# Kernel optimization log

Measured on AMD Instinct MI355X. Metric: run time of the kernel, lower is better.

Reference implementation:

```python
import jax, jax.numpy as jnp
import numpy as np

INPUT, HIDDEN, OUTPUT = 512, 512, 512


def setup_inputs() -> dict:
    key = jax.random.key(0)
    ks = jax.random.split(key, 8)
    B, T = 64, 1024
    s_x = 1.0 / np.sqrt(INPUT)
    s_h = 1.0 / np.sqrt(HIDDEN)
    return {
        "x": jax.random.normal(ks[0], (B, T, INPUT), jnp.float32),
        "h0": jnp.zeros((B, HIDDEN), jnp.float32),
        # nn.Linear params: weight (out, in), bias (out,), U(-1/sqrt(in), 1/sqrt(in))
        "W_xh": jax.random.uniform(ks[1], (HIDDEN, INPUT), jnp.float32, -s_x, s_x),
        "b_xh": jax.random.uniform(ks[2], (HIDDEN,), jnp.float32, -s_x, s_x),
        "W_hh": jax.random.uniform(ks[3], (HIDDEN, HIDDEN), jnp.float32, -s_h, s_h),
        "b_hh": jax.random.uniform(ks[4], (HIDDEN,), jnp.float32, -s_h, s_h),
        "W_hy": jax.random.uniform(ks[5], (OUTPUT, HIDDEN), jnp.float32, -s_h, s_h),
        "b_hy": jax.random.uniform(ks[6], (OUTPUT,), jnp.float32, -s_h, s_h),
    }


def reference(x, h0, W_xh, b_xh, W_hh, b_hh, W_hy, b_hy):
    # h_t = tanh(W_hh h_{t-1} + b_hh + W_xh x_t + b_xh); y_t = W_hy h_t + b_hy
    # Precompute the input projection for all timesteps (one big GEMM).
    xp = jnp.einsum("bti,hi->bth", x, W_xh) + b_xh + b_hh  # (B, T, H)

    def step(h, xp_t):
        h = jnp.tanh(h @ W_hh.T + xp_t)
        return h, h

    h_n, hs = jax.lax.scan(step, h0, jnp.swapaxes(xp, 0, 1))  # hs: (T, B, H)
    hs = jnp.swapaxes(hs, 0, 1)  # (B, T, H)
    output = jnp.einsum("bth,oh->bto", hs, W_hy) + b_hy
    return output, h_n
```

## Files before the change

kernel.cpp:

```cpp
#include <hip/hip_runtime.h>

typedef _Float16 f16;
typedef _Float16 f16x2 __attribute__((ext_vector_type(2)));
typedef _Float16 f16x4 __attribute__((ext_vector_type(4)));
typedef _Float16 f16x8 __attribute__((ext_vector_type(8)));
typedef float    f32x4 __attribute__((ext_vector_type(4)));

__device__ __forceinline__ int sdot4(int a, int b, int c) {
#if __has_builtin(__builtin_amdgcn_sdot4)
  return __builtin_amdgcn_sdot4(a, b, c, false);
#else
#pragma unroll
  for (int i = 0; i < 4; ++i)
    c += ((a << (24 - 8 * i)) >> 24) * ((b << (24 - 8 * i)) >> 24);
  return c;
#endif
}


__global__ void cvt_f32_to_f16(const float* __restrict__ in, f16* __restrict__ out, int n) {
  int i = (blockIdx.x * blockDim.x + threadIdx.x) * 4;
  if (i + 3 < n) {
    float4 v = *(const float4*)(in + i);
    f16x4 h; h[0] = (f16)v.x; h[1] = (f16)v.y; h[2] = (f16)v.z; h[3] = (f16)v.w;
    *(f16x4*)(out + i) = h;
  }
}

__global__ void bias_comb_kernel(const float* __restrict__ a, const float* __restrict__ b,
                                 float* __restrict__ o, int n) {
  int i = blockIdx.x * blockDim.x + threadIdx.x;
  if (i < n) o[i] = a[i] + b[i];
}

__global__ void zero_u32_kernel(unsigned* p) { *p = 0u; }

__global__ void wabsmax_kernel(const float* __restrict__ in, int n, unsigned* out) {
  float m = 0.f;
  for (int i = blockIdx.x * blockDim.x + threadIdx.x; i < n; i += gridDim.x * blockDim.x)
    m = fmaxf(m, fabsf(in[i]));
#pragma unroll
  for (int off = 32; off >= 1; off >>= 1)
    m = fmaxf(m, __shfl_xor(m, off));
  if ((threadIdx.x & 63) == 0) atomicMax(out, __float_as_uint(m));
}

__global__ void quant_w_kernel(const float* __restrict__ W, signed char* __restrict__ out,
                               const unsigned* __restrict__ wmax, int n) {
  float mx = __uint_as_float(*wmax);
  float inv = mx > 0.f ? 127.f / mx : 0.f;
  int i = (blockIdx.x * blockDim.x + threadIdx.x) * 4;
  if (i + 3 < n) {
    float4 v = *(const float4*)(W + i);
    int q0 = (int)__builtin_rintf(v.x * inv);
    int q1 = (int)__builtin_rintf(v.y * inv);
    int q2 = (int)__builtin_rintf(v.z * inv);
    int q3 = (int)__builtin_rintf(v.w * inv);
    unsigned p = (unsigned)(q0 & 255) | ((unsigned)(q1 & 255) << 8) |
                 ((unsigned)(q2 & 255) << 16) | ((unsigned)(q3 & 255) << 24);
    *(unsigned*)(out + i) = p;
  }
}


#define BM 128
#define BN 128
#define BKT 32
#define LDK 40

template <bool A_IS_F32>
__global__ __launch_bounds__(256, 2) void gemm_f16_kernel(
    const void* __restrict__ Aptr,
    const f16* __restrict__ B,
    const float* __restrict__ bias,
    float* __restrict__ C,
    int M, int N, int K) {
  __shared__ f16 As[BM][LDK];
  __shared__ f16 Bs[BN][LDK];

  const int tid = threadIdx.x;
  const int bm = blockIdx.y, bn = blockIdx.x;
  const int wave = tid >> 6, lane = tid & 63;
  const int wm = wave >> 1, wn = wave & 1;

  f32x4 acc[4][4] = {};

  for (int k0 = 0; k0 < K; k0 += BKT) {
#pragma unroll
    for (int it = 0; it < 2; ++it) {
      int idx = tid + it * 256;
      int row = idx >> 2;
      int kc  = (idx & 3) << 3;
      if (A_IS_F32) {
        const float* Af = (const float*)Aptr + (size_t)(bm * BM + row) * K + k0 + kc;
        float4 v0 = *(const float4*)Af;
        float4 v1 = *(const float4*)(Af + 4);
        f16x8 h;
        h[0] = (f16)v0.x; h[1] = (f16)v0.y; h[2] = (f16)v0.z; h[3] = (f16)v0.w;
        h[4] = (f16)v1.x; h[5] = (f16)v1.y; h[6] = (f16)v1.z; h[7] = (f16)v1.w;
        *(f16x8*)&As[row][kc] = h;
      } else {
        const f16* Ah = (const f16*)Aptr + (size_t)(bm * BM + row) * K + k0 + kc;
        *(f16x8*)&As[row][kc] = *(const f16x8*)Ah;
      }
      const f16* Bh = B + (size_t)(bn * BN + row) * K + k0 + kc;
      *(f16x8*)&Bs[row][kc] = *(const f16x8*)Bh;
    }
    __syncthreads();

    const int fr = lane & 15;
    const int fk = (lane >> 4) << 3;
    f16x8 af[4], bf[4];
#pragma unroll
    for (int i = 0; i < 4; ++i) af[i] = *(const f16x8*)&As[wm * 64 + i * 16 + fr][fk];
#pragma unroll
    for (int j = 0; j < 4; ++j) bf[j] = *(const f16x8*)&Bs[wn * 64 + j * 16 + fr][fk];
#pragma unroll
    for (int i = 0; i < 4; ++i)
#pragma unroll
      for (int j = 0; j < 4; ++j)
        acc[i][j] = __builtin_amdgcn_mfma_f32_16x16x32_f16(af[i], bf[j], acc[i][j], 0, 0, 0);
    __syncthreads();
  }

  const int fr = lane & 15;
  const int fq = lane >> 4;
#pragma unroll
  for (int i = 0; i < 4; ++i)
#pragma unroll
    for (int j = 0; j < 4; ++j)
#pragma unroll
      for (int r = 0; r < 4; ++r) {
        int row = bm * BM + wm * 64 + i * 16 + fq * 4 + r;
        int col = bn * BN + wn * 64 + j * 16 + fr;
        C[(size_t)row * N + col] = acc[i][j][r] + bias[col];
      }
}


#define RT 512

__global__ __launch_bounds__(RT, 1) void rnn_scan_kernel(
    const signed char* __restrict__ Whq,
    const unsigned* __restrict__ wmax,
    const float* __restrict__ h0,
    const float* __restrict__ xp,
    f16* __restrict__ hs,
    float* __restrict__ hn,
    int T) {
  __shared__ __align__(16) signed char hbuf[2][RT];
  const int tid = threadIdx.x;
  const int b   = blockIdx.x;

  const float qs = __uint_as_float(*wmax) * (1.0f / 16129.0f);

  const int* wrow = (const int*)(Whq + (size_t)tid * 512);
  int wq[128];
#pragma unroll
  for (int i = 0; i < 128; ++i) wq[i] = wrow[i];

  {
    float hv = h0[(size_t)b * 512 + tid];
    hv = fminf(1.f, fmaxf(-1.f, hv));
    hbuf[0][tid] = (signed char)(int)__builtin_rintf(127.f * hv);
  }
  __syncthreads();

  const float* xpb = xp + (size_t)b * T * 512 + tid;
  f16* hsb = hs + (size_t)b * T * 512 + tid;

  int cur = 0;
  float hlast = 0.f;
  float xv = xpb[0];
  for (int t = 0; t < T; ++t) {
    int tn = t + 1 < T ? t + 1 : t;
    float xn = xpb[(size_t)tn * 512];

    const int4* bcp = (const int4*)hbuf[cur];
    int a0 = 0, a1 = 0, a2 = 0, a3 = 0;
#pragma unroll
    for (int c = 0; c < 32; ++c) {
      int4 hv = bcp[c];
      a0 = sdot4(wq[4 * c + 0], hv.x, a0);
      a1 = sdot4(wq[4 * c + 1], hv.y, a1);
      a2 = sdot4(wq[4 * c + 2], hv.z, a2);
      a3 = sdot4(wq[4 * c + 3], hv.w, a3);
    }
    float acc = (float)((a0 + a1) + (a2 + a3)) * qs + xv;
    float e = __expf(2.0f * acc);
    float hnew = 1.0f - 2.0f * __builtin_amdgcn_rcpf(e + 1.0f);
    hlast = hnew;
    hsb[(size_t)t * 512] = (f16)hnew;
    hbuf[cur ^ 1][tid] = (signed char)(int)__builtin_rintf(127.f * hnew);
    __syncthreads();
    cur ^= 1;
    xv = xn;
  }
  hn[(size_t)b * 512 + tid] = hlast;
}


extern "C" void kernel_launch(void* const* d_in, const int* in_sizes, int n_in,
                              void* d_out, int out_size, void* d_ws, size_t ws_size,
                              hipStream_t stream) {
  const float* x    = (const float*)d_in[0];
  const float* h0   = (const float*)d_in[1];
  const float* W_xh = (const float*)d_in[2];
  const float* b_xh = (const float*)d_in[3];
  const float* W_hh = (const float*)d_in[4];
  const float* b_hh = (const float*)d_in[5];
  const float* W_hy = (const float*)d_in[6];
  const float* b_hy = (const float*)d_in[7];

  const int H = 512;
  const int B = in_sizes[1] / H;
  const int T = in_sizes[0] / (B * H);
  const int M = B * T;

  float* out = (float*)d_out;
  float* xpb = out;
  float* hn  = out + (size_t)M * H;

  char* w = (char*)d_ws;
  f16*         hsb    = (f16*)w;
  f16*         Wxh_h  = (f16*)(w + (size_t)M * H * 2);
  f16*         Why_h  = Wxh_h + H * H;
  signed char* Whq    = (signed char*)(Why_h + H * H);
  float*       biasc  = (float*)(Whq + H * H);
  unsigned*    wmax   = (unsigned*)(biasc + H);

  const int WN = H * H;
  cvt_f32_to_f16<<<WN / 1024, 256, 0, stream>>>(W_xh, Wxh_h, WN);
  cvt_f32_to_f16<<<WN / 1024, 256, 0, stream>>>(W_hy, Why_h, WN);
  bias_comb_kernel<<<2, 256, 0, stream>>>(b_xh, b_hh, biasc, H);

  zero_u32_kernel<<<1, 1, 0, stream>>>(wmax);
  wabsmax_kernel<<<64, 256, 0, stream>>>(W_hh, WN, wmax);
  quant_w_kernel<<<WN / 1024, 256, 0, stream>>>(W_hh, Whq, wmax, WN);

  gemm_f16_kernel<true><<<dim3(H / BN, M / BM), 256, 0, stream>>>(
      x, Wxh_h, biasc, xpb, M, H, H);

  rnn_scan_kernel<<<B, RT, 0, stream>>>(Whq, wmax, h0, xpb, hsb, hn, T);

  gemm_f16_kernel<false><<<dim3(H / BN, M / BM), 256, 0, stream>>>(
      hsb, Why_h, b_hy, out, M, H, H);
}
```

Measured before the change: 852.8 us.

## Split RNN scan K-dimension across two thread halves with LDS partial reduction

The recurrent scan block grows from 512 to 1024 threads, and each output neuron's 512-wide int8 dot product is split into two halves of 256. The upper half writes its partial sum to shared memory, and after a barrier the lower half adds it and computes the tanh update. This halves the serial sdot4 chain per step and the weight registers per thread (64 instead of 128), which allows more waves. The cost is an extra __syncthreads and an LDS round trip on every timestep of the latency-bound loop.

```diff
diff --git a/kernel.cpp b/kernel.cpp
--- a/kernel.cpp
+++ b/kernel.cpp
@@ -138,9 +138,18 @@
 }
 
 
-#define RT 512
-
-__global__ __launch_bounds__(RT, 1) void rnn_scan_kernel(
+#define ST 1024
+
+#define STEP_CHUNK(c, wa, wb, wcc, wd) \
+  { int4 hv = bcp[c];                  \
+    a0 = sdot4(wa, hv.x, a0);          \
+    a1 = sdot4(wb, hv.y, a1);          \
+    a2 = sdot4(wcc, hv.z, a2);         \
+    a3 = sdot4(wd, hv.w, a3); }
+
+__global__ __attribute__((amdgpu_flat_work_group_size(ST, ST),
+                          amdgpu_waves_per_eu(4, 4)))
+void rnn_scan_kernel(
     const signed char* __restrict__ Whq,
     const unsigned* __restrict__ wmax,
     const float* __restrict__ h0,
@@ -148,55 +157,98 @@
     f16* __restrict__ hs,
     float* __restrict__ hn,
     int T) {
-  __shared__ __align__(16) signed char hbuf[2][RT];
+  __shared__ __align__(16) signed char hbuf[2][512];
+  __shared__ int ipart[512];
+
   const int tid = threadIdx.x;
+  const int j   = tid & 511;
+  const int kh  = tid >> 9;
   const int b   = blockIdx.x;
 
   const float qs = __uint_as_float(*wmax) * (1.0f / 16129.0f);
 
-  const int* wrow = (const int*)(Whq + (size_t)tid * 512);
-  int wq[128];
-#pragma unroll
-  for (int i = 0; i < 128; ++i) wq[i] = wrow[i];
-
-  {
-    float hv = h0[(size_t)b * 512 + tid];
+  const int* wrow = (const int*)(Whq + (size_t)j * 512) + kh * 64;
+  int w0 =wrow[0],  w1 =wrow[1],  w2 =wrow[2],  w3 =wrow[3],
+      w4 =wrow[4],  w5 =wrow[5],  w6 =wrow[6],  w7 =wrow[7];
+  int w8 =wrow[8],  w9 =wrow[9],  w10=wrow[10], w11=wrow[11],
+      w12=wrow[12], w13=wrow[13], w14=wrow[14], w15=wrow[15];
+  int w16=wrow[16], w17=wrow[17], w18=wrow[18], w19=wrow[19],
+      w20=wrow[20], w21=wrow[21], w22=wrow[22], w23=wrow[23];
+  int w24=wrow[24], w25=wrow[25], w26=wrow[26], w27=wrow[27],
+      w28=wrow[28], w29=wrow[29], w30=wrow[30], w31=wrow[31];
+  int w32=wrow[32], w33=wrow[33], w34=wrow[34], w35=wrow[35],
+      w36=wrow[36], w37=wrow[37], w38=wrow[38], w39=wrow[39];
+  int w40=wrow[40], w41=wrow[41], w42=wrow[42], w43=wrow[43],
+      w44=wrow[44], w45=wrow[45], w46=wrow[46], w47=wrow[47];
+  int w48=wrow[48], w49=wrow[49], w50=wrow[50], w51=wrow[51],
+      w52=wrow[52], w53=wrow[53], w54=wrow[54], w55=wrow[55];
+  int w56=wrow[56], w57=wrow[57], w58=wrow[58], w59=wrow[59],
+      w60=wrow[60], w61=wrow[61], w62=wrow[62], w63=wrow[63];
+  asm volatile("" : "+v"(w0),"+v"(w1),"+v"(w2),"+v"(w3),"+v"(w4),"+v"(w5),"+v"(w6),"+v"(w7));
+  asm volatile("" : "+v"(w8),"+v"(w9),"+v"(w10),"+v"(w11),"+v"(w12),"+v"(w13),"+v"(w14),"+v"(w15));
+  asm volatile("" : "+v"(w16),"+v"(w17),"+v"(w18),"+v"(w19),"+v"(w20),"+v"(w21),"+v"(w22),"+v"(w23));
+  asm volatile("" : "+v"(w24),"+v"(w25),"+v"(w26),"+v"(w27),"+v"(w28),"+v"(w29),"+v"(w30),"+v"(w31));
+  asm volatile("" : "+v"(w32),"+v"(w33),"+v"(w34),"+v"(w35),"+v"(w36),"+v"(w37),"+v"(w38),"+v"(w39));
+  asm volatile("" : "+v"(w40),"+v"(w41),"+v"(w42),"+v"(w43),"+v"(w44),"+v"(w45),"+v"(w46),"+v"(w47));
+  asm volatile("" : "+v"(w48),"+v"(w49),"+v"(w50),"+v"(w51),"+v"(w52),"+v"(w53),"+v"(w54),"+v"(w55));
+  asm volatile("" : "+v"(w56),"+v"(w57),"+v"(w58),"+v"(w59),"+v"(w60),"+v"(w61),"+v"(w62),"+v"(w63));
+
+  if (kh == 0) {
+    float hv = h0[(size_t)b * 512 + j];
     hv = fminf(1.f, fmaxf(-1.f, hv));
-    hbuf[0][tid] = (signed char)(int)__builtin_rintf(127.f * hv);
+    hbuf[0][j] = (signed char)(int)__builtin_rintf(127.f * hv);
   }
   __syncthreads();
 
-  const float* xpb = xp + (size_t)b * T * 512 + tid;
-  f16* hsb = hs + (size_t)b * T * 512 + tid;
+  const float* xpb = xp + (size_t)b * T * 512 + j;
+  f16* hsb = hs + (size_t)b * T * 512 + j;
 
   int cur = 0;
   float hlast = 0.f;
-  float xv = xpb[0];
+  float xv = (kh == 0) ? xpb[0] : 0.f;
   for (int t = 0; t < T; ++t) {
-    int tn = t + 1 < T ? t + 1 : t;
-    float xn = xpb[(size_t)tn * 512];
-
-    const int4* bcp = (const int4*)hbuf[cur];
+    float xn = xv;
+    if (kh == 0) {
+      int tn = t + 1 < T ? t + 1 : t;
+      xn = xpb[(size_t)tn * 512];
+    }
+
+    const int4* bcp = (const int4*)hbuf[cur] + kh * 16;
     int a0 = 0, a1 = 0, a2 = 0, a3 = 0;
-#pragma unroll
-    for (int c = 0; c < 32; ++c) {
-      int4 hv = bcp[c];
-      a0 = sdot4(wq[4 * c + 0], hv.x, a0);
-      a1 = sdot4(wq[4 * c + 1], hv.y, a1);
-      a2 = sdot4(wq[4 * c + 2], hv.z, a2);
-      a3 = sdot4(wq[4 * c + 3], hv.w, a3);
+    STEP_CHUNK( 0, w0,  w1,  w2,  w3 )
+    STEP_CHUNK( 1, w4,  w5,  w6,  w7 )
+    STEP_CHUNK( 2, w8,  w9,  w10, w11)
+    STEP_CHUNK( 3, w12, w13, w14, w15)
+    STEP_CHUNK( 4, w16, w17, w18, w19)
+    STEP_CHUNK( 5, w20, w21, w22, w23)
+    STEP_CHUNK( 6, w24, w25, w26, w27)
+    STEP_CHUNK( 7, w28, w29, w30, w31)
+    STEP_CHUNK( 8, w32, w33, w34, w35)
+    STEP_CHUNK( 9, w36, w37, w38, w39)
+    STEP_CHUNK(10, w40, w41, w42, w43)
+    STEP_CHUNK(11, w44, w45, w46, w47)
+    STEP_CHUNK(12, w48, w49, w50, w51)
+    STEP_CHUNK(13, w52, w53, w54, w55)
+    STEP_CHUNK(14, w56, w57, w58, w59)
+    STEP_CHUNK(15, w60, w61, w62, w63)
+    int ai = (a0 + a1) + (a2 + a3);
+
+    if (kh == 1) ipart[j] = ai;
+    __syncthreads();
+
+    if (kh == 0) {
+      float acc = (float)(ai + ipart[j]) * qs + xv;
+      float e = __expf(2.0f * acc);
+      float hnew = 1.0f - 2.0f * __builtin_amdgcn_rcpf(e + 1.0f);
+      hlast = hnew;
+      hsb[(size_t)t * 512] = (f16)hnew;
+      hbuf[cur ^ 1][j] = (signed char)(int)__builtin_rintf(127.f * hnew);
     }
-    float acc = (float)((a0 + a1) + (a2 + a3)) * qs + xv;
-    float e = __expf(2.0f * acc);
-    float hnew = 1.0f - 2.0f * __builtin_amdgcn_rcpf(e + 1.0f);
-    hlast = hnew;
-    hsb[(size_t)t * 512] = (f16)hnew;
-    hbuf[cur ^ 1][tid] = (signed char)(int)__builtin_rintf(127.f * hnew);
     __syncthreads();
     cur ^= 1;
     xv = xn;
   }
-  hn[(size_t)b * 512 + tid] = hlast;
+  if (kh == 0) hn[(size_t)b * 512 + j] = hlast;
 }
 
 
@@ -241,7 +293,7 @@
   gemm_f16_kernel<true><<<dim3(H / BN, M / BM), 256, 0, stream>>>(
       x, Wxh_h, biasc, xpb, M, H, H);
 
-  rnn_scan_kernel<<<B, RT, 0, stream>>>(Whq, wmax, h0, xpb, hsb, hn, T);
+  rnn_scan_kernel<<<B, ST, 0, stream>>>(Whq, wmax, h0, xpb, hsb, hn, T);
 
   gemm_f16_kernel<false><<<dim3(H / BN, M / BM), 256, 0, stream>>>(
       hsb, Why_h, b_hy, out, M, H, H);
```

Measured after the change: 1.098 ms. +28.8%, slower.

## Use int8 MFMA for recurrent matvec in RNN scan kernel

Applied to the files above, without the earlier changes.

Replaces the per-thread sdot4 dot-product loop in the recurrent scan with v_mfma_i32_16x16x64_i8 instructions. Each wave keeps its slice of the quantized W_hh in AGPRs and reads the int8 hidden state from LDS as the A operand, broadcast across 16 rows. Only the first 16 lanes of each wave apply tanh and write outputs. Most of each MFMA tile is wasted because only one row is meaningful, and the hand-written s_nop hazard padding adds latency on every step.

```diff
diff --git a/kernel.cpp b/kernel.cpp
--- a/kernel.cpp
+++ b/kernel.cpp
@@ -5,17 +5,7 @@
 typedef _Float16 f16x4 __attribute__((ext_vector_type(4)));
 typedef _Float16 f16x8 __attribute__((ext_vector_type(8)));
 typedef float    f32x4 __attribute__((ext_vector_type(4)));
-
-__device__ __forceinline__ int sdot4(int a, int b, int c) {
-#if __has_builtin(__builtin_amdgcn_sdot4)
-  return __builtin_amdgcn_sdot4(a, b, c, false);
-#else
-#pragma unroll
-  for (int i = 0; i < 4; ++i)
-    c += ((a << (24 - 8 * i)) >> 24) * ((b << (24 - 8 * i)) >> 24);
-  return c;
-#endif
-}
+typedef int      intx4 __attribute__((ext_vector_type(4)));
 
 
 __global__ void cvt_f32_to_f16(const float* __restrict__ in, f16* __restrict__ out, int n) {
@@ -140,6 +130,17 @@
 
 #define RT 512
 
+#define MFMA(d, a, b) \
+  asm("v_mfma_i32_16x16x64_i8 %0, %1, %2, %0" : "+v"(d) : "v"(a), "a"(b))
+
+#define KSTEP(s) { intx4 av = ap[4 * (s)];       \
+    MFMA(d0, av, B##s##_0);                      \
+    MFMA(d1, av, B##s##_1);                      \
+    MFMA(d2, av, B##s##_2);                      \
+    MFMA(d3, av, B##s##_3); }
+
+#define BLD(s, nt) (*(const intx4*)(Whq + (size_t)(jb + (nt) * 16) * 512 + (s) * 64 + qoff))
+
 __global__ __launch_bounds__(RT, 1) void rnn_scan_kernel(
     const signed char* __restrict__ Whq,
     const unsigned* __restrict__ wmax,
@@ -148,16 +149,24 @@
     f16* __restrict__ hs,
     float* __restrict__ hn,
     int T) {
-  __shared__ __align__(16) signed char hbuf[2][RT];
-  const int tid = threadIdx.x;
-  const int b   = blockIdx.x;
+  __shared__ __align__(64) signed char hbuf[2][RT];
+  const int tid  = threadIdx.x;
+  const int lane = tid & 63;
+  const int w    = tid >> 6;
+  const int b    = blockIdx.x;
+  const int jb   = w * 64 + (lane & 15);
+  const int qoff = (lane >> 4) << 4;
 
   const float qs = __uint_as_float(*wmax) * (1.0f / 16129.0f);
 
-  const int* wrow = (const int*)(Whq + (size_t)tid * 512);
-  int wq[128];
-#pragma unroll
-  for (int i = 0; i < 128; ++i) wq[i] = wrow[i];
+  intx4 B0_0=BLD(0,0), B0_1=BLD(0,1), B0_2=BLD(0,2), B0_3=BLD(0,3);
+  intx4 B1_0=BLD(1,0), B1_1=BLD(1,1), B1_2=BLD(1,2), B1_3=BLD(1,3);
+  intx4 B2_0=BLD(2,0), B2_1=BLD(2,1), B2_2=BLD(2,2), B2_3=BLD(2,3);
+  intx4 B3_0=BLD(3,0), B3_1=BLD(3,1), B3_2=BLD(3,2), B3_3=BLD(3,3);
+  intx4 B4_0=BLD(4,0), B4_1=BLD(4,1), B4_2=BLD(4,2), B4_3=BLD(4,3);
+  intx4 B5_0=BLD(5,0), B5_1=BLD(5,1), B5_2=BLD(5,2), B5_3=BLD(5,3);
+  intx4 B6_0=BLD(6,0), B6_1=BLD(6,1), B6_2=BLD(6,2), B6_3=BLD(6,3);
+  intx4 B7_0=BLD(7,0), B7_1=BLD(7,1), B7_2=BLD(7,2), B7_3=BLD(7,3);
 
   {
     float hv = h0[(size_t)b * 512 + tid];
@@ -166,37 +175,54 @@
   }
   __syncthreads();
 
-  const float* xpb = xp + (size_t)b * T * 512 + tid;
-  f16* hsb = hs + (size_t)b * T * 512 + tid;
+  const float* xpb = xp + (size_t)b * T * 512 + jb;
+  f16* hsb = hs + (size_t)b * T * 512 + jb;
 
   int cur = 0;
-  float hlast = 0.f;
-  float xv = xpb[0];
+  float hl0 = 0.f, hl1 = 0.f, hl2 = 0.f, hl3 = 0.f;
+  float x0 = xpb[0], x1 = xpb[16], x2 = xpb[32], x3 = xpb[48];
+
   for (int t = 0; t < T; ++t) {
     int tn = t + 1 < T ? t + 1 : t;
-    float xn = xpb[(size_t)tn * 512];
-
-    const int4* bcp = (const int4*)hbuf[cur];
-    int a0 = 0, a1 = 0, a2 = 0, a3 = 0;
-#pragma unroll
-    for (int c = 0; c < 32; ++c) {
-      int4 hv = bcp[c];
-      a0 = sdot4(wq[4 * c + 0], hv.x, a0);
-      a1 = sdot4(wq[4 * c + 1], hv.y, a1);
-      a2 = sdot4(wq[4 * c + 2], hv.z, a2);
-      a3 = sdot4(wq[4 * c + 3], hv.w, a3);
+    size_t xo = (size_t)tn * 512;
+    float n0 = xpb[xo], n1 = xpb[xo + 16], n2 = xpb[xo + 32], n3 = xpb[xo + 48];
+
+    const intx4* ap = (const intx4*)(&hbuf[cur][0] + qoff);
+    intx4 d0 = {0, 0, 0, 0}, d1 = {0, 0, 0, 0}, d2 = {0, 0, 0, 0}, d3 = {0, 0, 0, 0};
+    KSTEP(0) KSTEP(1) KSTEP(2) KSTEP(3)
+    KSTEP(4) KSTEP(5) KSTEP(6) KSTEP(7)
+    asm volatile("s_nop 7\ns_nop 7" : "+v"(d0), "+v"(d1), "+v"(d2), "+v"(d3));
+
+    if (lane < 16) {
+      float y0 = (float)d0[0] * qs + x0;
+      float y1 = (float)d1[0] * qs + x1;
+      float y2 = (float)d2[0] * qs + x2;
+      float y3 = (float)d3[0] * qs + x3;
+      float e0 = __expf(2.f * y0), e1 = __expf(2.f * y1);
+      float e2 = __expf(2.f * y2), e3 = __expf(2.f * y3);
+      hl0 = 1.f - 2.f * __builtin_amdgcn_rcpf(e0 + 1.f);
+      hl1 = 1.f - 2.f * __builtin_amdgcn_rcpf(e1 + 1.f);
+      hl2 = 1.f - 2.f * __builtin_amdgcn_rcpf(e2 + 1.f);
+      hl3 = 1.f - 2.f * __builtin_amdgcn_rcpf(e3 + 1.f);
+      size_t ho = (size_t)t * 512;
+      hsb[ho] = (f16)hl0; hsb[ho + 16] = (f16)hl1;
+      hsb[ho + 32] = (f16)hl2; hsb[ho + 48] = (f16)hl3;
+      signed char* hbw = hbuf[cur ^ 1];
+      hbw[jb]      = (signed char)(int)__builtin_rintf(127.f * hl0);
+      hbw[jb + 16] = (signed char)(int)__builtin_rintf(127.f * hl1);
+      hbw[jb + 32] = (signed char)(int)__builtin_rintf(127.f * hl2);
+      hbw[jb + 48] = (signed char)(int)__builtin_rintf(127.f * hl3);
     }
-    float acc = (float)((a0 + a1) + (a2 + a3)) * qs + xv;
-    float e = __expf(2.0f * acc);
-    float hnew = 1.0f - 2.0f * __builtin_amdgcn_rcpf(e + 1.0f);
-    hlast = hnew;
-    hsb[(size_t)t * 512] = (f16)hnew;
-    hbuf[cur ^ 1][tid] = (signed char)(int)__builtin_rintf(127.f * hnew);
     __syncthreads();
     cur ^= 1;
-    xv = xn;
-  }
-  hn[(size_t)b * 512 + tid] = hlast;
+    x0 = n0; x1 = n1; x2 = n2; x3 = n3;
+  }
+  if (lane < 16) {
+    hn[(size_t)b * 512 + jb]      = hl0;
+    hn[(size_t)b * 512 + jb + 16] = hl1;
+    hn[(size_t)b * 512 + jb + 32] = hl2;
+    hn[(size_t)b * 512 + jb + 48] = hl3;
+  }
 }
 
 
```

New measurement: 1.009 ms. 1.18x slower.
